# Kernel tuning notes

Measured on AMD Instinct MI355X. Metric: run time of the kernel, lower is better.

The kernel has to match this reference:

```python
import jax, jax.numpy as jnp
import numpy as np

B, A, STATE_LEN, H, REL_LEN, E = 32, 64, 256, 128, 64, 16

def _mlp2(x, w1, b1, w2, b2):
    # DI-engine MLP, 2 layers, ReLU after every layer (incl. output)
    return jax.nn.relu(jax.nn.relu(x @ w1 + b1) @ w2 + b2)

def setup_inputs() -> dict:
    key = jax.random.key(0)
    ks = jax.random.split(key, 16)
    def w(k, fi, fo):
        return (jax.random.normal(k, (fi, fo), jnp.float32) / np.float32(np.sqrt(fi)))
    z = lambda n: jnp.zeros((n,), jnp.float32)
    return {
        "states": jax.random.normal(ks[0], (B, A, STATE_LEN), jnp.float32),
        "relations": jax.random.normal(ks[1], (B, A, A, REL_LEN), jnp.float32),
        "alive_mask": (jax.random.uniform(ks[2], (B, A)) > 0.3).astype(jnp.float32),
        "se_w1": w(ks[3], STATE_LEN, H), "se_b1": z(H),
        "se_w2": w(ks[4], H, H), "se_b2": z(H),
        "re_w1": w(ks[5], H + REL_LEN, H), "re_b1": z(H),
        "re_w2": w(ks[6], H, 2 * H), "re_b2": z(2 * H),
        "ra_w": w(ks[7], 3 * H, H), "ra_b": z(H),
        "ae_w1": w(ks[8], 4 * H, H), "ae_b1": z(H),
        "ae_w2": w(ks[9], H, 2 * H), "ae_b2": z(2 * H),
        "action_embed": jax.random.normal(ks[10], (E, H), jnp.float32) * np.float32(np.sqrt(2.0 / H)),
        "action_mask": jnp.ones((B, A, E + A), jnp.int32),
        "action": jax.random.randint(ks[11], (B,), 0, E + A),
        "agent_id": 0,
    }

def reference(states, relations, alive_mask,
              se_w1, se_b1, se_w2, se_b2,
              re_w1, re_b1, re_w2, re_b2,
              ra_w, ra_b,
              ae_w1, ae_b1, ae_w2, ae_b2,
              action_embed, action_mask, action, agent_id):
    del action_mask  # read by the torch module but never used
    b, a = states.shape[0], states.shape[1]
    h, e = se_w2.shape[1], action_embed.shape[0]
    # encode per-agent state: [B,A,H]
    s = _mlp2(states, se_w1, se_b1, se_w2, se_b2)
    # relation encoder: concat target-agent state onto each relation edge
    rel_in = jnp.concatenate(
        [relations, jnp.broadcast_to(s[:, None], (b, a, a, h))], axis=-1)
    r = _mlp2(rel_in, re_w1, re_b1, re_w2, re_b2)               # [B,A,A,2H]
    # relation aggregator: masked mean / masked max over source agents
    r_avr, r_max = jnp.split(r, 2, axis=-1)
    m = alive_mask[:, None, :, None]                             # [B,1,A,1]
    r_avr = (r_avr * m).mean(axis=-2)                            # [B,A,H]
    r_max = (r_max * m).max(axis=-2)                             # [B,A,H]
    s = jax.nn.relu(jnp.concatenate([s, r_avr, r_max], axis=-1) @ ra_w + ra_b)
    # pairwise action embeddings: [B,A,A,2H]
    ae_in = jnp.concatenate(
        [r,
         jnp.broadcast_to(s[:, None], (b, a, a, h)),
         jnp.broadcast_to(s[:, :, None], (b, a, a, h))], axis=-1)
    ae = _mlp2(ae_in, ae_w1, ae_b1, ae_w2, ae_b2)
    active, passive = jnp.split(ae, 2, axis=-1)                  # [B,A,A,H] each
    # acting agent `agent_id`: candidates = [embed_num self actions | A targeted actions]
    active_i = active[:, agent_id]                               # [B,A,H]
    active_full = jnp.concatenate(
        [jnp.broadcast_to(action_embed[None], (b, e, h)), active_i], axis=1)  # [B,E+A,H]
    sel = jnp.take_along_axis(active_full, action[:, None, None], axis=1)     # [B,1,H]
    state = s.at[:, agent_id].add(sel[:, 0])
    # passive side: target j receives passive embed iff action == E + j, else zero
    passive_i = passive[:, agent_id]                             # [B,A,H]
    hit = (action[:, None] == (e + jnp.arange(a))[None, :])      # [B,A]
    passive_sel = jnp.where(hit[:, :, None], passive_i, jnp.zeros((), states.dtype))
    state = state + passive_sel
    return state, sel[:, :, None], passive_sel
```

## Files before the change

### kernel.cpp

```cpp
#include <hip/hip_runtime.h>

#define NB 32
#define NA 64
#define SLEN 256
#define NH 128
#define RLEN 64
#define NE 16

typedef _Float16 f16;
typedef _Float16 f16x8 __attribute__((ext_vector_type(8)));
typedef _Float16 f16x4 __attribute__((ext_vector_type(4)));
typedef float f32x4 __attribute__((ext_vector_type(4)));

__device__ inline f16x8 cvt8(float4 a, float4 b) {
  f16x8 r;
  r[0] = (f16)a.x; r[1] = (f16)a.y; r[2] = (f16)a.z; r[3] = (f16)a.w;
  r[4] = (f16)b.x; r[5] = (f16)b.y; r[6] = (f16)b.z; r[7] = (f16)b.w;
  return r;
}

__device__ inline void gload_lds16(const float* g, float* l) {
  __builtin_amdgcn_global_load_lds((const __attribute__((address_space(1))) void*)g,
                                   (__attribute__((address_space(3))) void*)l, 16, 0, 0);
}

__device__ inline f16x8 gatherW(const float* __restrict__ W, int ld, int row0, int col) {
  f16x8 r;
#pragma unroll
  for (int t = 0; t < 8; ++t) r[t] = (f16)W[(size_t)(row0 + t) * ld + col];
  return r;
}

__global__ __launch_bounds__(256) void ka(const float* __restrict__ states,
                                          const float* __restrict__ se_w1,
                                          const float* __restrict__ se_b1,
                                          const float* __restrict__ se_w2,
                                          const float* __restrict__ se_b2,
                                          const float* __restrict__ re_w1,
                                          const float* __restrict__ re_b1,
                                          const float* __restrict__ re_w2,
                                          const float* __restrict__ ra_w,
                                          const float* __restrict__ ae_w1,
                                          const float* __restrict__ ae_w2,
                                          float* __restrict__ s_out,
                                          float* __restrict__ sp_pk,
                                          f16* __restrict__ pk) {
  __shared__ f16 t1[16 * 128];
  __shared__ f16 t2[16 * 128];
  if (blockIdx.x >= 128) {
    int t0 = (blockIdx.x - 128) * 256 + threadIdx.x;
    for (int idx = t0; idx < 188416; idx += 64 * 256) {
      const float* src; int ro, N, ld, base, dst;
      if (idx < 8192)        { src = re_w1; ro = 0;   N = 128; ld = 128; base = 0;      dst = 0; }
      else if (idx < 40960)  { src = re_w2; ro = 0;   N = 256; ld = 256; base = 8192;   dst = 8192; }
      else if (idx < 90112)  { src = ra_w;  ro = 0;   N = 128; ld = 128; base = 40960;  dst = 106496; }
      else if (idx < 106496) { src = ae_w1; ro = 256; N = 128; ld = 128; base = 90112;  dst = 155648; }
      else if (idx < 122880) { src = ae_w1; ro = 384; N = 128; ld = 128; base = 106496; dst = 172032; }
      else if (idx < 155648) { src = ae_w1; ro = 0;   N = 128; ld = 128; base = 122880; dst = 188416; }
      else                   { src = ae_w2; ro = 0;   N = 256; ld = 256; base = 155648; dst = 221184; }
      int li = idx - base;
      int t = li & 7, l = (li >> 3) & 63, rem = li >> 9;
      int NT = N >> 4;
      int nt = rem % NT, kt = rem / NT;
      int k = kt * 32 + (l >> 4) * 8 + t;
      int n = nt * 16 + (l & 15);
      pk[dst + li] = (f16)src[(size_t)(ro + k) * ld + n];
    }
    return;
  }
  const int row0 = blockIdx.x * 16;
  const int tid = threadIdx.x;
  const int w = tid >> 6, l = tid & 63, lr = l & 15, lh = l >> 4;

  f32x4 acc[2];
  acc[0] = (f32x4){0.f, 0.f, 0.f, 0.f};
  acc[1] = (f32x4){0.f, 0.f, 0.f, 0.f};

#pragma unroll
  for (int kt = 0; kt < 8; ++kt) {
    const float* p = states + (size_t)(row0 + lr) * SLEN + kt * 32 + lh * 8;
    f16x8 aF = cvt8(*(const float4*)p, *(const float4*)(p + 4));
#pragma unroll
    for (int n = 0; n < 2; ++n) {
      f16x8 bF = gatherW(se_w1, 128, kt * 32 + lh * 8, (w * 2 + n) * 16 + lr);
      acc[n] = __builtin_amdgcn_mfma_f32_16x16x32_f16(aF, bF, acc[n], 0, 0, 0);
    }
  }
#pragma unroll
  for (int n = 0; n < 2; ++n) {
    int h = w * 32 + n * 16 + lr;
    float bias = se_b1[h];
#pragma unroll
    for (int reg = 0; reg < 4; ++reg) {
      int j = lh * 4 + reg;
      float v = fmaxf(acc[n][reg] + bias, 0.f);
      unsigned off = (unsigned)((j * NH + h) * 2) ^ ((unsigned)(j & 7) << 4);
      *(f16*)((char*)t1 + off) = (f16)v;
    }
  }
  __syncthreads();

  acc[0] = (f32x4){0.f, 0.f, 0.f, 0.f};
  acc[1] = (f32x4){0.f, 0.f, 0.f, 0.f};
#pragma unroll
  for (int kt = 0; kt < 4; ++kt) {
    unsigned off = (unsigned)((lr * NH + kt * 32 + lh * 8) * 2) ^ ((unsigned)(lr & 7) << 4);
    f16x8 aF = *(const f16x8*)((char*)t1 + off);
#pragma unroll
    for (int n = 0; n < 2; ++n) {
      f16x8 bF = gatherW(se_w2, 128, kt * 32 + lh * 8, (w * 2 + n) * 16 + lr);
      acc[n] = __builtin_amdgcn_mfma_f32_16x16x32_f16(aF, bF, acc[n], 0, 0, 0);
    }
  }
#pragma unroll
  for (int n = 0; n < 2; ++n) {
    int h = w * 32 + n * 16 + lr;
    float bias = se_b2[h];
#pragma unroll
    for (int reg = 0; reg < 4; ++reg) {
      int j = lh * 4 + reg;
      float v = fmaxf(acc[n][reg] + bias, 0.f);
      s_out[(size_t)(row0 + j) * NH + h] = v;
      unsigned off = (unsigned)((j * NH + h) * 2) ^ ((unsigned)(j & 7) << 4);
      *(f16*)((char*)t2 + off) = (f16)v;
    }
  }
  __syncthreads();

  acc[0] = (f32x4){0.f, 0.f, 0.f, 0.f};
  acc[1] = (f32x4){0.f, 0.f, 0.f, 0.f};
#pragma unroll
  for (int kt = 0; kt < 4; ++kt) {
    unsigned off = (unsigned)((lr * NH + kt * 32 + lh * 8) * 2) ^ ((unsigned)(lr & 7) << 4);
    f16x8 aF = *(const f16x8*)((char*)t2 + off);
#pragma unroll
    for (int n = 0; n < 2; ++n) {
      f16x8 bF = gatherW(re_w1, 128, 64 + kt * 32 + lh * 8, (w * 2 + n) * 16 + lr);
      acc[n] = __builtin_amdgcn_mfma_f32_16x16x32_f16(aF, bF, acc[n], 0, 0, 0);
    }
  }
  const int bb = row0 >> 6;
  const int mtile = (row0 & 63) >> 4;
#pragma unroll
  for (int n = 0; n < 2; ++n) {
    int h = w * 32 + n * 16 + lr;
    float bias = re_b1[h];
    float4 outv;
#pragma unroll
    for (int reg = 0; reg < 4; ++reg) outv[reg] = acc[n][reg] + bias;
    *(float4*)(sp_pk + ((size_t)((bb * 4 + mtile) * 8 + w * 2 + n) * 64 + l) * 4) = outv;
  }
}

__global__ __launch_bounds__(256) void k3_rel(const float* __restrict__ relations,
                                              const float* __restrict__ alive_mask,
                                              const float* __restrict__ sp_pk,
                                              const float* __restrict__ re_b2,
                                              const f16* __restrict__ pw1,
                                              const f16* __restrict__ pw2,
                                              const int* __restrict__ agent_id,
                                              float* __restrict__ r_red,
                                              f16* __restrict__ r_agent) {
  __shared__ float relb[2][64 * 64];
  __shared__ f16 tl[64 * 128];
  __shared__ float alive[NA];
  const int bid = blockIdx.x;
  const int b = bid >> 4;
  const int i0 = (bid & 15) * 4;
  const int tid = threadIdx.x;
  const int w = tid >> 6, l = tid & 63, lr = l & 15, lh = l >> 4;

  auto stage = [&](int buf, int i) {
    const float* g = relations + (size_t)(b * NA + i) * NA * RLEN;
#pragma unroll
    for (int c4 = 0; c4 < 4; ++c4) {
      int c = w * 4 + c4;
      int srcf = c * 256 + ((l ^ ((4 * c + (l >> 4)) & 7)) * 4);
      gload_lds16(g + srcf, &relb[buf][c * 256]);
    }
  };

  stage(0, i0);
  if (tid < 64) alive[tid] = alive_mask[b * NA + tid];
  float bz[4];
#pragma unroll
  for (int n = 0; n < 4; ++n) bz[n] = re_b2[w * 64 + n * 16 + lr];
  f16x8 b1f[2][2];
#pragma unroll
  for (int kt = 0; kt < 2; ++kt)
#pragma unroll
    for (int n = 0; n < 2; ++n)
      b1f[kt][n] = *(const f16x8*)(pw1 + ((size_t)(kt * 8 + w * 2 + n) * 64 + l) * 8);
  float4 sp4[4][2];
  {
    const float* spp = sp_pk + (size_t)b * 8192;
#pragma unroll
    for (int mt = 0; mt < 4; ++mt)
#pragma unroll
      for (int n = 0; n < 2; ++n)
        sp4[mt][n] = *(const float4*)(spp + (size_t)((mt * 8 + w * 2 + n) * 64 + l) * 4);
  }
  const int aid = agent_id[0];
  const bool domax = (w >= 2);
  __syncthreads();

  for (int t = 0; t < 4; ++t) {
    const int cur = t & 1;
    f32x4 acc1[4][2];
#pragma unroll
    for (int mt = 0; mt < 4; ++mt)
#pragma unroll
      for (int n = 0; n < 2; ++n) acc1[mt][n] = (f32x4){0.f, 0.f, 0.f, 0.f};
#pragma unroll
    for (int mt = 0; mt < 4; ++mt) {
      int R = mt * 16 + lr;
      unsigned sw = ((unsigned)(R & 7)) << 4;
      f16x8 aK[2];
#pragma unroll
      for (int kt = 0; kt < 2; ++kt) {
        unsigned base = (unsigned)((R * 64 + kt * 32 + lh * 8) * 4);
        float4 v0 = *(const float4*)((char*)relb[cur] + (base ^ sw));
        float4 v1 = *(const float4*)((char*)relb[cur] + ((base + 16) ^ sw));
        aK[kt] = cvt8(v0, v1);
      }
#pragma unroll
      for (int kt = 0; kt < 2; ++kt)
#pragma unroll
        for (int n = 0; n < 2; ++n)
          acc1[mt][n] = __builtin_amdgcn_mfma_f32_16x16x32_f16(aK[kt], b1f[kt][n],
                                                               acc1[mt][n], 0, 0, 0);
    }
#pragma unroll
    for (int mt = 0; mt < 4; ++mt)
#pragma unroll
      for (int n = 0; n < 2; ++n) {
        int h = w * 32 + n * 16 + lr;
#pragma unroll
        for (int reg = 0; reg < 4; ++reg) {
          int j = mt * 16 + lh * 4 + reg;
          float v = fmaxf(acc1[mt][n][reg] + sp4[mt][n][reg], 0.f);
          unsigned off = (unsigned)((j * NH + h) * 2) ^ ((unsigned)(j & 7) << 4);
          *(f16*)((char*)tl + off) = (f16)v;
        }
      }
    __syncthreads();

    if (t < 3) stage(cur ^ 1, i0 + t + 1);

    f32x4 acc2[4][4];
#pragma unroll
    for (int mt = 0; mt < 4; ++mt)
#pragma unroll
      for (int n = 0; n < 4; ++n) acc2[mt][n] = (f32x4){0.f, 0.f, 0.f, 0.f};
#pragma unroll
    for (int kt2 = 0; kt2 < 4; ++kt2) {
      f16x8 a2[4];
#pragma unroll
      for (int mt = 0; mt < 4; ++mt) {
        int row = mt * 16 + lr;
        unsigned off = (unsigned)((row * 256 + kt2 * 64 + lh * 16)) ^ ((unsigned)(row & 7) << 4);
        a2[mt] = *(const f16x8*)((char*)tl + off);
      }
      f16x8 b2f[4];
#pragma unroll
      for (int n = 0; n < 4; ++n)
        b2f[n] = *(const f16x8*)(pw2 + ((size_t)(kt2 * 16 + w * 4 + n) * 64 + l) * 8);
#pragma unroll
      for (int mt = 0; mt < 4; ++mt)
#pragma unroll
        for (int n = 0; n < 4; ++n)
          acc2[mt][n] = __builtin_amdgcn_mfma_f32_16x16x32_f16(a2[mt], b2f[n], acc2[mt][n], 0, 0, 0);
    }

    const int i = i0 + t;
    const bool isagent = (i == aid);
    float red[4];
#pragma unroll
    for (int n = 0; n < 4; ++n) red[n] = 0.f;
#pragma unroll
    for (int n = 0; n < 4; ++n) {
      int col = w * 64 + n * 16 + lr;
      float bias = bz[n];
#pragma unroll
      for (int mt = 0; mt < 4; ++mt)
#pragma unroll
        for (int reg = 0; reg < 4; ++reg) {
          int j = mt * 16 + lh * 4 + reg;
          float rv = fmaxf(acc2[mt][n][reg] + bias, 0.f);
          float rm = rv * alive[j];
          red[n] = domax ? fmaxf(red[n], rm) : (red[n] + rm);
          if (isagent) r_agent[((size_t)b * NA + j) * 256 + col] = (f16)rv;
        }
    }
#pragma unroll
    for (int n = 0; n < 4; ++n) {
      float v = red[n];
      float v1 = __shfl_xor(v, 16, 64);
      v = domax ? fmaxf(v, v1) : v + v1;
      float v2 = __shfl_xor(v, 32, 64);
      v = domax ? fmaxf(v, v2) : v + v2;
      if (lh == 0) r_red[(size_t)(b * NA + i) * 256 + w * 64 + n * 16 + lr] = v;
    }
    __syncthreads();
  }
}

__global__ __launch_bounds__(256) void k4m(const float* __restrict__ s,
                                           const float* __restrict__ r_red,
                                           const float* __restrict__ ra_b,
                                           const f16* __restrict__ pra,
                                           float* __restrict__ s_new) {
  __shared__ f16 x3[16 * 384];
  const int row0 = blockIdx.x * 16;
  const int tid = threadIdx.x;
  const int w = tid >> 6, l = tid & 63, lr = l & 15, lh = l >> 4;

#pragma unroll
  for (int it = 0; it < 6; ++it) {
    int e = it * 1024 + tid * 4;
    int row = e / 384;
    int c = e - row * 384;
    float4 v;
    if (c < 128) {
      v = *(const float4*)(s + (size_t)(row0 + row) * NH + c);
    } else {
      v = *(const float4*)(r_red + (size_t)(row0 + row) * 256 + (c - 128));
      if (c < 256) { v.x *= (1.f / 64.f); v.y *= (1.f / 64.f); v.z *= (1.f / 64.f); v.w *= (1.f / 64.f); }
    }
    f16x4 hv;
    hv[0] = (f16)v.x; hv[1] = (f16)v.y; hv[2] = (f16)v.z; hv[3] = (f16)v.w;
    unsigned off = (unsigned)((row * 384 + c) * 2) ^ ((unsigned)(row & 7) << 4);
    *(f16x4*)((char*)x3 + off) = hv;
  }
  __syncthreads();

  f32x4 acc[2];
  acc[0] = (f32x4){0.f, 0.f, 0.f, 0.f};
  acc[1] = (f32x4){0.f, 0.f, 0.f, 0.f};
#pragma unroll
  for (int kt = 0; kt < 12; ++kt) {
    unsigned off = (unsigned)((lr * 384 + kt * 32 + lh * 8) * 2) ^ ((unsigned)(lr & 7) << 4);
    f16x8 aF = *(const f16x8*)((char*)x3 + off);
#pragma unroll
    for (int n = 0; n < 2; ++n) {
      f16x8 bF = *(const f16x8*)(pra + ((size_t)(kt * 8 + w * 2 + n) * 64 + l) * 8);
      acc[n] = __builtin_amdgcn_mfma_f32_16x16x32_f16(aF, bF, acc[n], 0, 0, 0);
    }
  }
#pragma unroll
  for (int n = 0; n < 2; ++n) {
    int h = w * 32 + n * 16 + lr;
    float bias = ra_b[h];
#pragma unroll
    for (int reg = 0; reg < 4; ++reg) {
      int j = lh * 4 + reg;
      s_new[(size_t)(row0 + j) * NH + h] = fmaxf(acc[n][reg] + bias, 0.f);
    }
  }
}

__global__ __launch_bounds__(256) void k5mg(const f16* __restrict__ r_agent,
                                            const float* __restrict__ s_new,
                                            const float* __restrict__ ae_b1,
                                            const float* __restrict__ ae_b2,
                                            const float* __restrict__ action_embed,
                                            const int* __restrict__ action,
                                            const int* __restrict__ agent_id,
                                            const f16* __restrict__ pae1a,
                                            const f16* __restrict__ pae1b,
                                            const f16* __restrict__ pae1c,
                                            const f16* __restrict__ pae2,
                                            float* __restrict__ out_state,
                                            float* __restrict__ out_sel,
                                            float* __restrict__ out_passive) {
  __shared__ f16 xa[16 * 512];
  __shared__ f16 t1[16 * 128];
  __shared__ float selL[16][128];
  __shared__ float pasL[16][128];
  __shared__ int actL[16];
  const int aid = agent_id[0];
  const int tid = threadIdx.x;

  if (blockIdx.x >= 2) {
    int q = (blockIdx.x - 2) * 256 + tid;
    int idx = q * 4;
    int h = idx & 127;
    int row = idx >> 7;
    int b = row >> 6, i = row & 63;
    int act = action[b];
    bool special = (i == aid) || (act >= NE && i == act - NE);
    if (!special) {
      *(float4*)(out_state + idx) = *(const float4*)(s_new + idx);
      *(float4*)(out_passive + idx) = (float4){0.f, 0.f, 0.f, 0.f};
    }
    (void)h;
    return;
  }

  const int b0 = blockIdx.x * 16;
  const int w = tid >> 6, l = tid & 63, lr = l & 15, lh = l >> 4;

  {
    int row = tid & 15, g = tid >> 4;
    int bb = b0 + row;
    int act = action[bb];
    if (g == 0) actL[row] = act;
    int jj = act >= NE ? act - NE : 0;
    int k0 = g * 32;
    f16x8 vv[4];
    if (g < 8) {
      const f16* src = r_agent + ((size_t)bb * NA + jj) * 256 + k0;
#pragma unroll
      for (int c = 0; c < 4; ++c) vv[c] = *(const f16x8*)(src + c * 8);
    } else {
      const float* src = (g < 12) ? (s_new + ((size_t)bb * NA + jj) * NH + (g - 8) * 32)
                                  : (s_new + ((size_t)bb * NA + aid) * NH + (g - 12) * 32);
#pragma unroll
      for (int c = 0; c < 4; ++c)
        vv[c] = cvt8(*(const float4*)(src + c * 8), *(const float4*)(src + c * 8 + 4));
    }
#pragma unroll
    for (int c = 0; c < 4; ++c) {
      unsigned off = (unsigned)((row * 512 + k0 + c * 8) * 2) ^ ((unsigned)(row & 7) << 4);
      *(f16x8*)((char*)xa + off) = vv[c];
    }
  }
  __syncthreads();

  f32x4 acc[2];
  acc[0] = (f32x4){0.f, 0.f, 0.f, 0.f};
  acc[1] = (f32x4){0.f, 0.f, 0.f, 0.f};
#pragma unroll
  for (int kt = 0; kt < 16; ++kt) {
    unsigned off = (unsigned)((lr * 512 + kt * 32 + lh * 8) * 2) ^ ((unsigned)(lr & 7) << 4);
    f16x8 aF = *(const f16x8*)((char*)xa + off);
    const f16* pseg = (kt < 8) ? pae1a : (kt < 12) ? pae1b : pae1c;
    int ktl = (kt < 8) ? kt : (kt < 12) ? kt - 8 : kt - 12;
#pragma unroll
    for (int n = 0; n < 2; ++n) {
      f16x8 bF = *(const f16x8*)(pseg + ((size_t)(ktl * 8 + w * 2 + n) * 64 + l) * 8);
      acc[n] = __builtin_amdgcn_mfma_f32_16x16x32_f16(aF, bF, acc[n], 0, 0, 0);
    }
  }
#pragma unroll
  for (int n = 0; n < 2; ++n) {
    int h = w * 32 + n * 16 + lr;
    float bias = ae_b1[h];
#pragma unroll
    for (int reg = 0; reg < 4; ++reg) {
      int j = lh * 4 + reg;
      float v = fmaxf(acc[n][reg] + bias, 0.f);
      unsigned off = (unsigned)((j * NH + h) * 2) ^ ((unsigned)(j & 7) << 4);
      *(f16*)((char*)t1 + off) = (f16)v;
    }
  }
  __syncthreads();

  f32x4 acc2[4];
#pragma unroll
  for (int n = 0; n < 4; ++n) acc2[n] = (f32x4){0.f, 0.f, 0.f, 0.f};
#pragma unroll
  for (int kt = 0; kt < 4; ++kt) {
    unsigned off = (unsigned)((lr * NH + kt * 32 + lh * 8) * 2) ^ ((unsigned)(lr & 7) << 4);
    f16x8 aF = *(const f16x8*)((char*)t1 + off);
#pragma unroll
    for (int n = 0; n < 4; ++n) {
      f16x8 bF = *(const f16x8*)(pae2 + ((size_t)(kt * 16 + w * 4 + n) * 64 + l) * 8);
      acc2[n] = __builtin_amdgcn_mfma_f32_16x16x32_f16(aF, bF, acc2[n], 0, 0, 0);
    }
  }
#pragma unroll
  for (int n = 0; n < 4; ++n) {
    int col = w * 64 + n * 16 + lr;
    float bias = ae_b2[col];
#pragma unroll
    for (int reg = 0; reg < 4; ++reg) {
      int row = lh * 4 + reg;
      int act = actL[row];
      float v = fmaxf(acc2[n][reg] + bias, 0.f);
      if (col < NH) {
        selL[row][col] = (act < NE) ? action_embed[act * NH + col] : v;
      } else {
        pasL[row][col - NH] = (act < NE) ? 0.f : v;
      }
    }
  }
  __syncthreads();

  for (int e = tid; e < 16 * 128; e += 256) {
    int rb = e >> 7, c = e & 127;
    int bb = b0 + rb;
    int act = actL[rb];
    float sv = selL[rb][c], pv = pasL[rb][c];
    out_sel[bb * NH + c] = sv;
    size_t ia = ((size_t)bb * NA + aid) * NH + c;
    bool paid = (act >= NE) && (act - NE == aid);
    out_state[ia] = s_new[ia] + sv + (paid ? pv : 0.f);
    out_passive[ia] = paid ? pv : 0.f;
    if (act >= NE && act - NE != aid) {
      size_t ip = ((size_t)bb * NA + (act - NE)) * NH + c;
      out_state[ip] = s_new[ip] + pv;
      out_passive[ip] = pv;
    }
  }
}

extern "C" void kernel_launch(void* const* d_in, const int* in_sizes, int n_in,
                              void* d_out, int out_size, void* d_ws, size_t ws_size,
                              hipStream_t stream) {
  (void)in_sizes; (void)n_in; (void)out_size; (void)ws_size;
  const float* states       = (const float*)d_in[0];
  const float* relations    = (const float*)d_in[1];
  const float* alive_mask   = (const float*)d_in[2];
  const float* se_w1        = (const float*)d_in[3];
  const float* se_b1        = (const float*)d_in[4];
  const float* se_w2        = (const float*)d_in[5];
  const float* se_b2        = (const float*)d_in[6];
  const float* re_w1        = (const float*)d_in[7];
  const float* re_b1        = (const float*)d_in[8];
  const float* re_w2        = (const float*)d_in[9];
  const float* re_b2        = (const float*)d_in[10];
  const float* ra_w         = (const float*)d_in[11];
  const float* ra_b         = (const float*)d_in[12];
  const float* ae_w1        = (const float*)d_in[13];
  const float* ae_b1        = (const float*)d_in[14];
  const float* ae_w2        = (const float*)d_in[15];
  const float* ae_b2        = (const float*)d_in[16];
  const float* action_embed = (const float*)d_in[17];
  const int*   action       = (const int*)d_in[19];
  const int*   agent_id     = (const int*)d_in[20];
  float* out = (float*)d_out;

  float* wsf     = (float*)d_ws;
  float* s       = wsf;
  float* sp_pk   = wsf + 262144;
  float* r_red   = wsf + 524288;
  float* s_new   = wsf + 1048576;
  f16*   wsh     = (f16*)(wsf + 1318912);
  f16*   r_agent = wsh;
  f16*   pk      = wsh + 524288;
  f16*   pw_re1a = pk;
  f16*   pw_re2  = pk + 8192;
  f16*   pw_ra   = pk + 106496;
  f16*   pw_ae1b = pk + 155648;
  f16*   pw_ae1c = pk + 172032;
  f16*   pw_ae1a = pk + 188416;
  f16*   pw_ae2  = pk + 221184;

  ka<<<192, 256, 0, stream>>>(states, se_w1, se_b1, se_w2, se_b2, re_w1, re_b1,
                              re_w2, ra_w, ae_w1, ae_w2, s, sp_pk, pk);
  k3_rel<<<512, 256, 0, stream>>>(relations, alive_mask, sp_pk, re_b2, pw_re1a, pw_re2,
                                  agent_id, r_red, r_agent);
  k4m<<<128, 256, 0, stream>>>(s, r_red, ra_b, pw_ra, s_new);
  k5mg<<<258, 256, 0, stream>>>(r_agent, s_new, ae_b1, ae_b2, action_embed, action,
                                agent_id, pw_ae1a, pw_ae1b, pw_ae1c, pw_ae2,
                                out, out + 262144, out + 266240);
}
```

Before: 170.9 us.

## Pre-convert relations to fp16 and split relation kernel to one row per block

Adds 512 extra blocks to the first kernel that convert the fp32 relations tensor into an fp16 workspace copy. The relation kernel then reads fp16 directly into registers as MFMA operands, and processes one source row per block across 2048 blocks. This replaces the previous double-buffered LDS staging over four rows per block. The aim is to halve the relation kernel's read bytes and raise parallelism, at the cost of an extra full read and write pass over relations and per-block reloading of weights and sp terms.

Measured after the change: 167.4 us. -2.1%, faster.

```diff
diff --git a/kernel.cpp b/kernel.cpp
--- a/kernel.cpp
+++ b/kernel.cpp
@@ -19,11 +19,6 @@
   return r;
 }
 
-__device__ inline void gload_lds16(const float* g, float* l) {
-  __builtin_amdgcn_global_load_lds((const __attribute__((address_space(1))) void*)g,
-                                   (__attribute__((address_space(3))) void*)l, 16, 0, 0);
-}
-
 __device__ inline f16x8 gatherW(const float* __restrict__ W, int ld, int row0, int col) {
   f16x8 r;
 #pragma unroll
@@ -32,6 +27,7 @@
 }
 
 __global__ __launch_bounds__(256) void ka(const float* __restrict__ states,
+                                          const float* __restrict__ relations,
                                           const float* __restrict__ se_w1,
                                           const float* __restrict__ se_b1,
                                           const float* __restrict__ se_w2,
@@ -44,9 +40,24 @@
                                           const float* __restrict__ ae_w2,
                                           float* __restrict__ s_out,
                                           float* __restrict__ sp_pk,
-                                          f16* __restrict__ pk) {
+                                          f16* __restrict__ pk,
+                                          f16* __restrict__ rel16) {
   __shared__ f16 t1[16 * 128];
   __shared__ f16 t2[16 * 128];
+  if (blockIdx.x >= 192) {
+    const int cb = blockIdx.x - 192;
+    const float4* r4 = (const float4*)relations;
+    f16x4* o4 = (f16x4*)rel16;
+#pragma unroll
+    for (int it = 0; it < 16; ++it) {
+      int i4 = cb * 4096 + it * 256 + threadIdx.x;
+      float4 v = r4[i4];
+      f16x4 h;
+      h[0] = (f16)v.x; h[1] = (f16)v.y; h[2] = (f16)v.z; h[3] = (f16)v.w;
+      o4[i4] = h;
+    }
+    return;
+  }
   if (blockIdx.x >= 128) {
     int t0 = (blockIdx.x - 128) * 256 + threadIdx.x;
     for (int idx = t0; idx < 188416; idx += 64 * 256) {
@@ -152,7 +163,7 @@
   }
 }
 
-__global__ __launch_bounds__(256) void k3_rel(const float* __restrict__ relations,
+__global__ __launch_bounds__(256) void k3_rel(const f16* __restrict__ rel16,
                                               const float* __restrict__ alive_mask,
                                               const float* __restrict__ sp_pk,
                                               const float* __restrict__ re_b2,
@@ -161,30 +172,25 @@
                                               const int* __restrict__ agent_id,
                                               float* __restrict__ r_red,
                                               f16* __restrict__ r_agent) {
-  __shared__ float relb[2][64 * 64];
   __shared__ f16 tl[64 * 128];
   __shared__ float alive[NA];
   const int bid = blockIdx.x;
-  const int b = bid >> 4;
-  const int i0 = (bid & 15) * 4;
+  const int b = bid >> 6, i = bid & 63;
   const int tid = threadIdx.x;
   const int w = tid >> 6, l = tid & 63, lr = l & 15, lh = l >> 4;
 
-  auto stage = [&](int buf, int i) {
-    const float* g = relations + (size_t)(b * NA + i) * NA * RLEN;
-#pragma unroll
-    for (int c4 = 0; c4 < 4; ++c4) {
-      int c = w * 4 + c4;
-      int srcf = c * 256 + ((l ^ ((4 * c + (l >> 4)) & 7)) * 4);
-      gload_lds16(g + srcf, &relb[buf][c * 256]);
-    }
-  };
-
-  stage(0, i0);
   if (tid < 64) alive[tid] = alive_mask[b * NA + tid];
   float bz[4];
 #pragma unroll
   for (int n = 0; n < 4; ++n) bz[n] = re_b2[w * 64 + n * 16 + lr];
+
+  const f16* rp = rel16 + (size_t)bid * (NA * RLEN);
+  f16x8 a1[4][2];
+#pragma unroll
+  for (int mt = 0; mt < 4; ++mt)
+#pragma unroll
+    for (int kt = 0; kt < 2; ++kt)
+      a1[mt][kt] = *(const f16x8*)(rp + (mt * 16 + lr) * RLEN + kt * 32 + lh * 8);
   f16x8 b1f[2][2];
 #pragma unroll
   for (int kt = 0; kt < 2; ++kt)
@@ -200,108 +206,90 @@
       for (int n = 0; n < 2; ++n)
         sp4[mt][n] = *(const float4*)(spp + (size_t)((mt * 8 + w * 2 + n) * 64 + l) * 4);
   }
+
+  f32x4 acc1[4][2];
+#pragma unroll
+  for (int mt = 0; mt < 4; ++mt)
+#pragma unroll
+    for (int n = 0; n < 2; ++n) acc1[mt][n] = (f32x4){0.f, 0.f, 0.f, 0.f};
+#pragma unroll
+  for (int kt = 0; kt < 2; ++kt)
+#pragma unroll
+    for (int mt = 0; mt < 4; ++mt)
+#pragma unroll
+      for (int n = 0; n < 2; ++n)
+        acc1[mt][n] = __builtin_amdgcn_mfma_f32_16x16x32_f16(a1[mt][kt], b1f[kt][n],
+                                                             acc1[mt][n], 0, 0, 0);
+
+#pragma unroll
+  for (int mt = 0; mt < 4; ++mt)
+#pragma unroll
+    for (int n = 0; n < 2; ++n) {
+      int h = w * 32 + n * 16 + lr;
+#pragma unroll
+      for (int reg = 0; reg < 4; ++reg) {
+        int j = mt * 16 + lh * 4 + reg;
+        float v = fmaxf(acc1[mt][n][reg] + sp4[mt][n][reg], 0.f);
+        unsigned off = (unsigned)((j * NH + h) * 2) ^ ((unsigned)(j & 7) << 4);
+        *(f16*)((char*)tl + off) = (f16)v;
+      }
+    }
+  __syncthreads();
+
+  f32x4 acc2[4][4];
+#pragma unroll
+  for (int mt = 0; mt < 4; ++mt)
+#pragma unroll
+    for (int n = 0; n < 4; ++n) acc2[mt][n] = (f32x4){0.f, 0.f, 0.f, 0.f};
+#pragma unroll
+  for (int kt2 = 0; kt2 < 4; ++kt2) {
+    f16x8 a2[4];
+#pragma unroll
+    for (int mt = 0; mt < 4; ++mt) {
+      int row = mt * 16 + lr;
+      unsigned off = (unsigned)((row * 256 + kt2 * 64 + lh * 16)) ^ ((unsigned)(row & 7) << 4);
+      a2[mt] = *(const f16x8*)((char*)tl + off);
+    }
+    f16x8 b2f[4];
+#pragma unroll
+    for (int n = 0; n < 4; ++n)
+      b2f[n] = *(const f16x8*)(pw2 + ((size_t)(kt2 * 16 + w * 4 + n) * 64 + l) * 8);
+#pragma unroll
+    for (int mt = 0; mt < 4; ++mt)
+#pragma unroll
+      for (int n = 0; n < 4; ++n)
+        acc2[mt][n] = __builtin_amdgcn_mfma_f32_16x16x32_f16(a2[mt], b2f[n], acc2[mt][n], 0, 0, 0);
+  }
+
   const int aid = agent_id[0];
+  const bool isagent = (i == aid);
   const bool domax = (w >= 2);
-  __syncthreads();
-
-  for (int t = 0; t < 4; ++t) {
-    const int cur = t & 1;
-    f32x4 acc1[4][2];
+  float red[4];
+#pragma unroll
+  for (int n = 0; n < 4; ++n) red[n] = 0.f;
+#pragma unroll
+  for (int n = 0; n < 4; ++n) {
+    int col = w * 64 + n * 16 + lr;
+    float bias = bz[n];
 #pragma unroll
     for (int mt = 0; mt < 4; ++mt)
 #pragma unroll
-      for (int n = 0; n < 2; ++n) acc1[mt][n] = (f32x4){0.f, 0.f, 0.f, 0.f};
-#pragma unroll
-    for (int mt = 0; mt < 4; ++mt) {
-      int R = mt * 16 + lr;
-      unsigned sw = ((unsigned)(R & 7)) << 4;
-      f16x8 aK[2];
-#pragma unroll
-      for (int kt = 0; kt < 2; ++kt) {
-        unsigned base = (unsigned)((R * 64 + kt * 32 + lh * 8) * 4);
-        float4 v0 = *(const float4*)((char*)relb[cur] + (base ^ sw));
-        float4 v1 = *(const float4*)((char*)relb[cur] + ((base + 16) ^ sw));
-        aK[kt] = cvt8(v0, v1);
+      for (int reg = 0; reg < 4; ++reg) {
+        int j = mt * 16 + lh * 4 + reg;
+        float rv = fmaxf(acc2[mt][n][reg] + bias, 0.f);
+        float rm = rv * alive[j];
+        red[n] = domax ? fmaxf(red[n], rm) : (red[n] + rm);
+        if (isagent) r_agent[((size_t)b * NA + j) * 256 + col] = (f16)rv;
       }
-#pragma unroll
-      for (int kt = 0; kt < 2; ++kt)
-#pragma unroll
-        for (int n = 0; n < 2; ++n)
-          acc1[mt][n] = __builtin_amdgcn_mfma_f32_16x16x32_f16(aK[kt], b1f[kt][n],
-                                                               acc1[mt][n], 0, 0, 0);
-    }
-#pragma unroll
-    for (int mt = 0; mt < 4; ++mt)
-#pragma unroll
-      for (int n = 0; n < 2; ++n) {
-        int h = w * 32 + n * 16 + lr;
-#pragma unroll
-        for (int reg = 0; reg < 4; ++reg) {
-          int j = mt * 16 + lh * 4 + reg;
-          float v = fmaxf(acc1[mt][n][reg] + sp4[mt][n][reg], 0.f);
-          unsigned off = (unsigned)((j * NH + h) * 2) ^ ((unsigned)(j & 7) << 4);
-          *(f16*)((char*)tl + off) = (f16)v;
-        }
-      }
-    __syncthreads();
-
-    if (t < 3) stage(cur ^ 1, i0 + t + 1);
-
-    f32x4 acc2[4][4];
-#pragma unroll
-    for (int mt = 0; mt < 4; ++mt)
-#pragma unroll
-      for (int n = 0; n < 4; ++n) acc2[mt][n] = (f32x4){0.f, 0.f, 0.f, 0.f};
-#pragma unroll
-    for (int kt2 = 0; kt2 < 4; ++kt2) {
-      f16x8 a2[4];
-#pragma unroll
-      for (int mt = 0; mt < 4; ++mt) {
-        int row = mt * 16 + lr;
-        unsigned off = (unsigned)((row * 256 + kt2 * 64 + lh * 16)) ^ ((unsigned)(row & 7) << 4);
-        a2[mt] = *(const f16x8*)((char*)tl + off);
-      }
-      f16x8 b2f[4];
-#pragma unroll
-      for (int n = 0; n < 4; ++n)
-        b2f[n] = *(const f16x8*)(pw2 + ((size_t)(kt2 * 16 + w * 4 + n) * 64 + l) * 8);
-#pragma unroll
-      for (int mt = 0; mt < 4; ++mt)
-#pragma unroll
-        for (int n = 0; n < 4; ++n)
-          acc2[mt][n] = __builtin_amdgcn_mfma_f32_16x16x32_f16(a2[mt], b2f[n], acc2[mt][n], 0, 0, 0);
-    }
-
-    const int i = i0 + t;
-    const bool isagent = (i == aid);
-    float red[4];
-#pragma unroll
-    for (int n = 0; n < 4; ++n) red[n] = 0.f;
-#pragma unroll
-    for (int n = 0; n < 4; ++n) {
-      int col = w * 64 + n * 16 + lr;
-      float bias = bz[n];
-#pragma unroll
-      for (int mt = 0; mt < 4; ++mt)
-#pragma unroll
-        for (int reg = 0; reg < 4; ++reg) {
-          int j = mt * 16 + lh * 4 + reg;
-          float rv = fmaxf(acc2[mt][n][reg] + bias, 0.f);
-          float rm = rv * alive[j];
-          red[n] = domax ? fmaxf(red[n], rm) : (red[n] + rm);
-          if (isagent) r_agent[((size_t)b * NA + j) * 256 + col] = (f16)rv;
-        }
-    }
-#pragma unroll
-    for (int n = 0; n < 4; ++n) {
-      float v = red[n];
-      float v1 = __shfl_xor(v, 16, 64);
-      v = domax ? fmaxf(v, v1) : v + v1;
-      float v2 = __shfl_xor(v, 32, 64);
-      v = domax ? fmaxf(v, v2) : v + v2;
-      if (lh == 0) r_red[(size_t)(b * NA + i) * 256 + w * 64 + n * 16 + lr] = v;
-    }
-    __syncthreads();
+  }
+#pragma unroll
+  for (int n = 0; n < 4; ++n) {
+    float v = red[n];
+    float v1 = __shfl_xor(v, 16, 64);
+    v = domax ? fmaxf(v, v1) : v + v1;
+    float v2 = __shfl_xor(v, 32, 64);
+    v = domax ? fmaxf(v, v2) : v + v2;
+    if (lh == 0) r_red[(size_t)bid * 256 + w * 64 + n * 16 + lr] = v;
   }
 }
 
@@ -384,7 +372,6 @@
   if (blockIdx.x >= 2) {
     int q = (blockIdx.x - 2) * 256 + tid;
     int idx = q * 4;
-    int h = idx & 127;
     int row = idx >> 7;
     int b = row >> 6, i = row & 63;
     int act = action[b];
@@ -393,7 +380,6 @@
       *(float4*)(out_state + idx) = *(const float4*)(s_new + idx);
       *(float4*)(out_passive + idx) = (float4){0.f, 0.f, 0.f, 0.f};
     }
-    (void)h;
     return;
   }
 
@@ -539,6 +525,7 @@
   f16*   wsh     = (f16*)(wsf + 1318912);
   f16*   r_agent = wsh;
   f16*   pk      = wsh + 524288;
+  f16*   rel16   = wsh + 524288 + 253952;
   f16*   pw_re1a = pk;
   f16*   pw_re2  = pk + 8192;
   f16*   pw_ra   = pk + 106496;
@@ -547,10 +534,11 @@
   f16*   pw_ae1a = pk + 188416;
   f16*   pw_ae2  = pk + 221184;
 
-  ka<<<192, 256, 0, stream>>>(states, se_w1, se_b1, se_w2, se_b2, re_w1, re_b1,
-                              re_w2, ra_w, ae_w1, ae_w2, s, sp_pk, pk);
-  k3_rel<<<512, 256, 0, stream>>>(relations, alive_mask, sp_pk, re_b2, pw_re1a, pw_re2,
-                                  agent_id, r_red, r_agent);
+  ka<<<704, 256, 0, stream>>>(states, relations, se_w1, se_b1, se_w2, se_b2,
+                              re_w1, re_b1, re_w2, ra_w, ae_w1, ae_w2,
+                              s, sp_pk, pk, rel16);
+  k3_rel<<<2048, 256, 0, stream>>>(rel16, alive_mask, sp_pk, re_b2, pw_re1a, pw_re2,
+                                   agent_id, r_red, r_agent);
   k4m<<<128, 256, 0, stream>>>(s, r_red, ra_b, pw_ra, s_new);
   k5mg<<<258, 256, 0, stream>>>(r_agent, s_new, ae_b1, ae_b2, action_embed, action,
                                 agent_id, pw_ae1a, pw_ae1b, pw_ae1c, pw_ae2,
```
